# Optimization experiments

Hardware: AMD Instinct MI355X
Metric: run time of the kernel (lower is better)

Reference implementation:

```python
import jax, jax.numpy as jnp
import numpy as np

N_NODES = 100000
N_EDGES = 1600000
F_IN, HID, N_CLS = 64, 64, 40
K = 3  # Chebyshev order


def setup_inputs() -> dict:
    key = jax.random.key(0)
    k = jax.random.split(key, 7)
    x = jax.random.normal(k[0], (N_NODES, F_IN), dtype=jnp.float32)
    edge_index = jax.random.randint(k[1], (2, N_EDGES), 0, N_NODES, dtype=jnp.int32)
    W1 = jax.random.normal(k[2], (K, F_IN, HID), dtype=jnp.float32) * 0.05
    b1 = jax.random.normal(k[3], (HID,), dtype=jnp.float32) * 0.05
    W2 = jax.random.normal(k[4], (K, HID, N_CLS), dtype=jnp.float32) * 0.05
    b2 = jax.random.normal(k[5], (N_CLS,), dtype=jnp.float32) * 0.05
    return {"x": x, "edge_index": edge_index, "W1": W1, "b1": b1, "W2": W2, "b2": b2}


def _norm(edge_index, n):
    # PyG ChebConv with sym normalization and lambda_max=2.0:
    # L_hat edge weight = -deg^{-1/2}[src] * deg^{-1/2}[dst]; self-loop weight 0.
    src, dst = edge_index[0], edge_index[1]
    keep = (src != dst).astype(jnp.float32)  # remove_self_loops
    deg = jax.ops.segment_sum(keep, src, num_segments=n)
    dis = jnp.where(deg > 0, 1.0 / jnp.sqrt(jnp.maximum(deg, 1.0)), 0.0)
    w = -dis[src] * dis[dst] * keep
    return src, dst, w


def _spmm(x, src, dst, w, n):
    # out[i] = sum_{e: dst[e]==i} w[e] * x[src[e]]
    return jax.ops.segment_sum(w[:, None] * x[src], dst, num_segments=n)


def _cheb_conv(x, src, dst, w, W, b, n):
    Tx0 = x
    out = Tx0 @ W[0]
    Tx1 = _spmm(x, src, dst, w, n)
    out = out + Tx1 @ W[1]
    for k in range(2, W.shape[0]):
        Tx2 = 2.0 * _spmm(Tx1, src, dst, w, n) - Tx0
        out = out + Tx2 @ W[k]
        Tx0, Tx1 = Tx1, Tx2
    return out + b


def reference(x, edge_index, W1, b1, W2, b2):
    n = x.shape[0]
    src, dst, w = _norm(edge_index, n)
    h = jax.nn.relu(_cheb_conv(x, src, dst, w, W1, b1, n))
    out = _cheb_conv(h, src, dst, w, W2, b2, n)
    return jax.nn.softmax(out, axis=1)
```

## Files before the change

### kernel.cpp

```cpp
#include <hip/hip_runtime.h>
#include <hip/hip_fp16.h>

#define N_NODES 100000
#define N_EDGES 1600000
#define NCLS 40
#define NBUCK 196
#define CAPE 8960
#define CAPC 10752
#define DUMMY N_NODES

typedef unsigned short u16;
typedef unsigned int u32;
typedef short bf16x8 __attribute__((ext_vector_type(8)));
typedef float f32x4 __attribute__((ext_vector_type(4)));

static inline size_t align256(size_t x) { return (x + 255) & ~(size_t)255; }

__device__ __forceinline__ float bf2f(u16 h) { return __uint_as_float(((u32)h) << 16); }
__device__ __forceinline__ u16 f2bf(float f) {
    u32 u = __float_as_uint(f);
    u += 0x7FFFu + ((u >> 16) & 1u);
    return (u16)(u >> 16);
}
__device__ __forceinline__ u32 pk2(u16 a, u16 b) { return (u32)a | ((u32)b << 16); }
__device__ __forceinline__ u32 pack15(float f) {
    return ((u32)__half_as_ushort(__float2half(f))) & 0x7FFFu;
}
__device__ __forceinline__ float unpack15(u32 bits) {
    return __half2float(__ushort_as_half((u16)bits));
}
__device__ __forceinline__ int perm16(int r, int c8) {
    int base16 = (c8 >> 4) << 4;
    if (r < base16) {
        int b = r >> 4, w = r & 15;
        return (b << 4) + ((w & 1) << 3) + (w >> 1);
    }
    int w = r - base16;
    return base16 + ((w & 1) << 2) + (w >> 1);
}

#define PS_BLOCKS 391
#define CONV_BLOCKS 6250

__global__ __launch_bounds__(256) void pscatter_conv(const int* __restrict__ src,
                                                     const int* __restrict__ dst,
                                                     int* __restrict__ gFillD,
                                                     int* __restrict__ gFillS,
                                                     u32* __restrict__ partD,
                                                     u16* __restrict__ partS,
                                                     const float* __restrict__ x,
                                                     u16* __restrict__ xb) {
    if (blockIdx.x >= PS_BLOCKS) {
        int i = (blockIdx.x - PS_BLOCKS) * 256 + threadIdx.x;
        float4 v = *(const float4*)(x + (size_t)i * 4);
        ushort4 o;
        o.x = f2bf(v.x); o.y = f2bf(v.y); o.z = f2bf(v.z); o.w = f2bf(v.w);
        *(ushort4*)(xb + (size_t)i * 4) = o;
        return;
    }
    __shared__ int histD[NBUCK], histS[NBUCK], chunkD[NBUCK], chunkS[NBUCK];
    int tid = threadIdx.x;
    int base = blockIdx.x * 4096;

    int4 sv[4], dv[4];
#pragma unroll
    for (int j = 0; j < 4; ++j) {
        int idx = base + j * 1024 + tid * 4;
        if (idx < N_EDGES) {
            sv[j] = *(const int4*)(src + idx);
            dv[j] = *(const int4*)(dst + idx);
        } else {
            sv[j] = make_int4(0, 0, 0, 0);
            dv[j] = make_int4(0, 0, 0, 0);
        }
    }

    for (int i = tid; i < NBUCK; i += 256) { histD[i] = 0; histS[i] = 0; }
    __syncthreads();
#pragma unroll
    for (int j = 0; j < 4; ++j)
#pragma unroll
        for (int k = 0; k < 4; ++k) {
            int s = ((const int*)&sv[j])[k], d = ((const int*)&dv[j])[k];
            if (s != d) {
                atomicAdd(&histD[d >> 9], 1);
                atomicAdd(&histS[s >> 9], 1);
            }
        }
    __syncthreads();
    for (int B = tid; B < NBUCK; B += 256) {
        int cD = histD[B];
        chunkD[B] = cD ? atomicAdd(&gFillD[B], cD) : 0;
        int cS = histS[B];
        chunkS[B] = cS ? atomicAdd(&gFillS[B], cS) : 0;
    }
    __syncthreads();
    for (int i = tid; i < NBUCK; i += 256) { histD[i] = 0; histS[i] = 0; }
    __syncthreads();
#pragma unroll
    for (int j = 0; j < 4; ++j)
#pragma unroll
        for (int k = 0; k < 4; ++k) {
            int s = ((const int*)&sv[j])[k], d = ((const int*)&dv[j])[k];
            if (s != d) {
                int bD = d >> 9;
                int r = atomicAdd(&histD[bD], 1);
                int o = chunkD[bD] + r;
                if (o < CAPE) partD[bD * CAPE + o] = ((u32)s << 9) | (u32)(d & 511);
                int bS = s >> 9;
                int r2 = atomicAdd(&histS[bS], 1);
                int o2 = chunkS[bS] + r2;
                if (o2 < CAPE) partS[bS * CAPE + o2] = (u16)(s & 511);
            }
        }
}

__global__ __launch_bounds__(256) void build_dis(const u16* __restrict__ partS,
                                                 const int* __restrict__ gFillS,
                                                 float* __restrict__ dis) {
    __shared__ int cnt[512];
    int tid = threadIdx.x;
    int B = blockIdx.x;
    for (int i = tid; i < 512; i += 256) cnt[i] = 0;
    __syncthreads();
    int nS = min(gFillS[B], CAPE);
    for (int i = tid; i < nS; i += 256) atomicAdd(&cnt[partS[B * CAPE + i]], 1);
    __syncthreads();
    for (int n = tid; n < 512; n += 256) {
        int node = B * 512 + n;
        if (node < N_NODES) {
            int dg = cnt[n];
            dis[node] = dg > 0 ? 1.0f / sqrtf((float)dg) : 0.0f;
        }
    }
}

__global__ __launch_bounds__(256) void build_csr(const u32* __restrict__ partD,
                                                 const int* __restrict__ gFillD,
                                                 const float* __restrict__ dis,
                                                 u32* __restrict__ csr,
                                                 int2* __restrict__ meta) {
    __shared__ int cnt[512], loc[512], rnk[512];
    int tid = threadIdx.x;
    int B = blockIdx.x;
    for (int i = tid; i < 512; i += 256) { cnt[i] = 0; rnk[i] = 0; }
    __syncthreads();
    int nD = min(gFillD[B], CAPE);
    for (int i = tid; i < nD; i += 256) atomicAdd(&cnt[partD[B * CAPE + i] & 511], 1);
    __syncthreads();
    if (tid < 64) {
        int bb = tid * 8, c8[8], mysum = 0;
#pragma unroll
        for (int j = 0; j < 8; ++j) { c8[j] = (cnt[bb + j] + 7) & ~7; mysum += c8[j]; }
        int incl = mysum;
#pragma unroll
        for (int off = 1; off < 64; off <<= 1) {
            int v = __shfl_up(incl, off);
            if (tid >= off) incl += v;
        }
        int run = incl - mysum;
#pragma unroll
        for (int j = 0; j < 8; ++j) { loc[bb + j] = run; run += c8[j]; }
    }
    __syncthreads();
    for (int n = tid; n < 512; n += 256) {
        int node = B * 512 + n;
        if (node < N_NODES) {
            int c = cnt[n], c8 = (c + 7) & ~7;
            meta[node] = make_int2(B * CAPC + loc[n], c);
            for (int e = c; e < c8; ++e)
                csr[B * CAPC + loc[n] + perm16(e, c8)] = (u32)DUMMY;
        }
    }
    for (int i = tid; i < nD; i += 256) {
        u32 p = partD[B * CAPE + i];
        int ln = p & 511;
        u32 s = p >> 9;
        int r = atomicAdd(&rnk[ln], 1);
        int c8 = (cnt[ln] + 7) & ~7;
        int pos = loc[ln] + perm16(r, c8);
        if (pos < CAPC) csr[B * CAPC + pos] = s | (pack15(dis[s]) << 17);
    }
}

__global__ __launch_bounds__(256) void spmm(const u16* __restrict__ in,
                                            const float* __restrict__ dis,
                                            const int2* __restrict__ meta,
                                            const u32* __restrict__ csr,
                                            u16* __restrict__ outhi,
                                            u16* __restrict__ outlo) {
    int node = (blockIdx.x * 256 + threadIdx.x) >> 6;
    int lane = threadIdx.x & 63;
    if (node >= N_NODES) return;
    node = __builtin_amdgcn_readfirstlane(node);
    int2 mt = meta[node];
    int c8 = (mt.y + 7) & ~7;
    const u32* lst = csr + mt.x;
    const u32* in32 = (const u32*)in;
    const int hsel = lane >> 5;
    const int fl = lane & 31;
    float acc0 = 0.0f, acc1 = 0.0f;
    int e = 0;
    for (; e + 16 <= c8; e += 16) {
        const u32* half = lst + e + (hsel << 3);
        uint4 ea = *(const uint4*)half;
        uint4 eb = *(const uint4*)(half + 4);
        u32 e0 = ea.x, e1 = ea.y, e2 = ea.z, e3 = ea.w;
        u32 e4 = eb.x, e5 = eb.y, e6 = eb.z, e7 = eb.w;
        u32 v0 = in32[((e0 & 0x1FFFFu) << 5) + fl];
        u32 v1 = in32[((e1 & 0x1FFFFu) << 5) + fl];
        u32 v2 = in32[((e2 & 0x1FFFFu) << 5) + fl];
        u32 v3 = in32[((e3 & 0x1FFFFu) << 5) + fl];
        u32 v4 = in32[((e4 & 0x1FFFFu) << 5) + fl];
        u32 v5 = in32[((e5 & 0x1FFFFu) << 5) + fl];
        u32 v6 = in32[((e6 & 0x1FFFFu) << 5) + fl];
        u32 v7 = in32[((e7 & 0x1FFFFu) << 5) + fl];
        float w0 = unpack15(e0 >> 17), w1 = unpack15(e1 >> 17);
        float w2 = unpack15(e2 >> 17), w3 = unpack15(e3 >> 17);
        float w4 = unpack15(e4 >> 17), w5 = unpack15(e5 >> 17);
        float w6 = unpack15(e6 >> 17), w7 = unpack15(e7 >> 17);
        acc0 = fmaf(w0, __uint_as_float(v0 << 16), acc0);
        acc1 = fmaf(w0, __uint_as_float(v0 & 0xFFFF0000u), acc1);
        acc0 = fmaf(w1, __uint_as_float(v1 << 16), acc0);
        acc1 = fmaf(w1, __uint_as_float(v1 & 0xFFFF0000u), acc1);
        acc0 = fmaf(w2, __uint_as_float(v2 << 16), acc0);
        acc1 = fmaf(w2, __uint_as_float(v2 & 0xFFFF0000u), acc1);
        acc0 = fmaf(w3, __uint_as_float(v3 << 16), acc0);
        acc1 = fmaf(w3, __uint_as_float(v3 & 0xFFFF0000u), acc1);
        acc0 = fmaf(w4, __uint_as_float(v4 << 16), acc0);
        acc1 = fmaf(w4, __uint_as_float(v4 & 0xFFFF0000u), acc1);
        acc0 = fmaf(w5, __uint_as_float(v5 << 16), acc0);
        acc1 = fmaf(w5, __uint_as_float(v5 & 0xFFFF0000u), acc1);
        acc0 = fmaf(w6, __uint_as_float(v6 << 16), acc0);
        acc1 = fmaf(w6, __uint_as_float(v6 & 0xFFFF0000u), acc1);
        acc0 = fmaf(w7, __uint_as_float(v7 << 16), acc0);
        acc1 = fmaf(w7, __uint_as_float(v7 & 0xFFFF0000u), acc1);
    }
    if (e < c8) {
        const u32* half = lst + e + (hsel << 2);
        uint4 ea = *(const uint4*)half;
        u32 e0 = ea.x, e1 = ea.y, e2 = ea.z, e3 = ea.w;
        u32 v0 = in32[((e0 & 0x1FFFFu) << 5) + fl];
        u32 v1 = in32[((e1 & 0x1FFFFu) << 5) + fl];
        u32 v2 = in32[((e2 & 0x1FFFFu) << 5) + fl];
        u32 v3 = in32[((e3 & 0x1FFFFu) << 5) + fl];
        float w0 = unpack15(e0 >> 17), w1 = unpack15(e1 >> 17);
        float w2 = unpack15(e2 >> 17), w3 = unpack15(e3 >> 17);
        acc0 = fmaf(w0, __uint_as_float(v0 << 16), acc0);
        acc1 = fmaf(w0, __uint_as_float(v0 & 0xFFFF0000u), acc1);
        acc0 = fmaf(w1, __uint_as_float(v1 << 16), acc0);
        acc1 = fmaf(w1, __uint_as_float(v1 & 0xFFFF0000u), acc1);
        acc0 = fmaf(w2, __uint_as_float(v2 << 16), acc0);
        acc1 = fmaf(w2, __uint_as_float(v2 & 0xFFFF0000u), acc1);
        acc0 = fmaf(w3, __uint_as_float(v3 << 16), acc0);
        acc1 = fmaf(w3, __uint_as_float(v3 & 0xFFFF0000u), acc1);
    }
    acc0 += __shfl_xor(acc0, 32);
    acc1 += __shfl_xor(acc1, 32);
    float vd = -dis[node];
    float f0 = vd * acc0, f1 = vd * acc1;
    u32 o32 = ((u32)node << 5) + fl;
    u16 h0 = f2bf(f0), h1 = f2bf(f1);
    if (hsel == 0) {
        ((u32*)outhi)[o32] = pk2(h0, h1);
    } else {
        ((u32*)outlo)[o32] = pk2(f2bf(f0 - bf2f(h0)), f2bf(f1 - bf2f(h1)));
    }
}

#define DGRID 1250
#define DNT 5
#define LSTR 200

__device__ __forceinline__ float foldW(const float* __restrict__ W, int kk, int col,
                                       int ncols) {
    float wv = W[kk * ncols + col];
    if (kk < 64) wv -= W[(kk + 128) * ncols + col];
    else if (kk >= 128) wv += wv;
    return wv;
}

__global__ __launch_bounds__(256) void dense1_mf(const float* __restrict__ x,
                                                 const u16* __restrict__ a1h,
                                                 const u16* __restrict__ a1l,
                                                 const u16* __restrict__ tyh,
                                                 const u16* __restrict__ tyl,
                                                 const float* __restrict__ W,
                                                 const float* __restrict__ bias,
                                                 u16* __restrict__ ohi,
                                                 u16* __restrict__ olo) {
    __shared__ u16 Ah[16 * LSTR], Al[16 * LSTR];
    const int tid = threadIdx.x, wid = tid >> 6, lane = tid & 63;
    const int lrow = lane & 15, lk8 = (lane >> 4) * 8;
    const int col = wid * 16 + lrow;

    bf16x8 wh[6], wl[6];
#pragma unroll
    for (int c = 0; c < 6; ++c) {
        bf16x8 h, l;
#pragma unroll
        for (int i = 0; i < 8; ++i) {
            float wv = foldW(W, c * 32 + lk8 + i, col, 64);
            u16 hb_ = f2bf(wv);
            h[i] = (short)hb_;
            l[i] = (short)f2bf(wv - bf2f(hb_));
        }
        wh[c] = h; wl[c] = l;
    }
    float bv = bias[col];
    const int srow = tid >> 4, sc4 = (tid & 15) * 4;

    for (int t = 0; t < DNT; ++t) {
        int r0 = (blockIdx.x * DNT + t) * 16;
        size_t rb = ((size_t)(r0 + srow) << 6) + sc4;
        {
            float4 v = *(const float4*)&x[rb];
            const float* vp = (const float*)&v;
            ushort4 hv, lv;
#pragma unroll
            for (int i = 0; i < 4; ++i) {
                u16 hb_ = f2bf(vp[i]);
                ((u16*)&hv)[i] = hb_;
                ((u16*)&lv)[i] = f2bf(vp[i] - bf2f(hb_));
            }
            *(ushort4*)&Ah[srow * LSTR + sc4] = hv;
            *(ushort4*)&Al[srow * LSTR + sc4] = lv;
        }
        *(ushort4*)&Ah[srow * LSTR + 64 + sc4] = *(const ushort4*)&a1h[rb];
        *(ushort4*)&Al[srow * LSTR + 64 + sc4] = *(const ushort4*)&a1l[rb];
        *(ushort4*)&Ah[srow * LSTR + 128 + sc4] = *(const ushort4*)&tyh[rb];
        *(ushort4*)&Al[srow * LSTR + 128 + sc4] = *(const ushort4*)&tyl[rb];
        __syncthreads();

        f32x4 acc = {bv, bv, bv, bv};
#pragma unroll
        for (int c = 0; c < 6; ++c) {
            bf16x8 ah = *(const bf16x8*)&Ah[lrow * LSTR + c * 32 + lk8];
            bf16x8 al = *(const bf16x8*)&Al[lrow * LSTR + c * 32 + lk8];
            acc = __builtin_amdgcn_mfma_f32_16x16x32_bf16(ah, wh[c], acc, 0, 0, 0);
            acc = __builtin_amdgcn_mfma_f32_16x16x32_bf16(al, wh[c], acc, 0, 0, 0);
            acc = __builtin_amdgcn_mfma_f32_16x16x32_bf16(ah, wl[c], acc, 0, 0, 0);
        }
        __syncthreads();

#pragma unroll
        for (int j = 0; j < 4; ++j) {
            int row = r0 + (lane >> 4) * 4 + j;
            float v = fmaxf(acc[j], 0.0f);
            u16 hb_ = f2bf(v);
            ohi[((size_t)row << 6) + col] = hb_;
            olo[((size_t)row << 6) + col] = f2bf(v - bf2f(hb_));
        }
    }
}

__global__ __launch_bounds__(256) void dense2_mf(const u16* __restrict__ a0h,
                                                 const u16* __restrict__ a0l,
                                                 const u16* __restrict__ a1h,
                                                 const u16* __restrict__ a1l,
                                                 const u16* __restrict__ tyh,
                                                 const u16* __restrict__ tyl,
                                                 const float* __restrict__ W,
                                                 const float* __restrict__ bias,
                                                 float* __restrict__ out) {
    __shared__ u16 Ah[16 * LSTR], Al[16 * LSTR];
    __shared__ float Ls[16][48];
    const int tid = threadIdx.x, wid = tid >> 6, lane = tid & 63;
    const int lrow = lane & 15, lk8 = (lane >> 4) * 8;
    const int col = wid * 16 + lrow;
    const bool act = (wid < 3);
    const bool cok = act && (col < NCLS);

    bf16x8 wh[6], wl[6];
#pragma unroll
    for (int c = 0; c < 6; ++c) {
        bf16x8 h = 0, l = 0;
        if (cok) {
#pragma unroll
            for (int i = 0; i < 8; ++i) {
                float wv = foldW(W, c * 32 + lk8 + i, col, NCLS);
                u16 hb_ = f2bf(wv);
                h[i] = (short)hb_;
                l[i] = (short)f2bf(wv - bf2f(hb_));
            }
        }
        wh[c] = h; wl[c] = l;
    }
    float bv = cok ? bias[col] : 0.0f;
    const int srow = tid >> 4, sc4 = (tid & 15) * 4;

    for (int t = 0; t < DNT; ++t) {
        int r0 = (blockIdx.x * DNT + t) * 16;
        size_t rb = ((size_t)(r0 + srow) << 6) + sc4;
        *(ushort4*)&Ah[srow * LSTR + sc4] = *(const ushort4*)&a0h[rb];
        *(ushort4*)&Al[srow * LSTR + sc4] = *(const ushort4*)&a0l[rb];
        *(ushort4*)&Ah[srow * LSTR + 64 + sc4] = *(const ushort4*)&a1h[rb];
        *(ushort4*)&Al[srow * LSTR + 64 + sc4] = *(const ushort4*)&a1l[rb];
        *(ushort4*)&Ah[srow * LSTR + 128 + sc4] = *(const ushort4*)&tyh[rb];
        *(ushort4*)&Al[srow * LSTR + 128 + sc4] = *(const ushort4*)&tyl[rb];
        __syncthreads();

        if (act) {
            f32x4 acc = {bv, bv, bv, bv};
#pragma unroll
            for (int c = 0; c < 6; ++c) {
                bf16x8 ah = *(const bf16x8*)&Ah[lrow * LSTR + c * 32 + lk8];
                bf16x8 al = *(const bf16x8*)&Al[lrow * LSTR + c * 32 + lk8];
                acc = __builtin_amdgcn_mfma_f32_16x16x32_bf16(ah, wh[c], acc, 0, 0, 0);
                acc = __builtin_amdgcn_mfma_f32_16x16x32_bf16(al, wh[c], acc, 0, 0, 0);
                acc = __builtin_amdgcn_mfma_f32_16x16x32_bf16(ah, wl[c], acc, 0, 0, 0);
            }
#pragma unroll
            for (int j = 0; j < 4; ++j) Ls[(lane >> 4) * 4 + j][col] = acc[j];
        }
        __syncthreads();

        {
            int row = wid * 4 + (lane >> 4);
            int cg = lane & 15;
            float v0 = Ls[row][cg];
            float v1 = Ls[row][cg + 16];
            float v2 = (cg < 8) ? Ls[row][cg + 32] : -1e30f;
            float m = fmaxf(fmaxf(v0, v1), v2);
#pragma unroll
            for (int o = 8; o; o >>= 1) m = fmaxf(m, __shfl_xor(m, o));
            float e0 = expf(v0 - m), e1 = expf(v1 - m);
            float e2 = (cg < 8) ? expf(v2 - m) : 0.0f;
            float s = e0 + e1 + e2;
#pragma unroll
            for (int o = 8; o; o >>= 1) s += __shfl_xor(s, o);
            float inv = 1.0f / s;
            size_t ob = (size_t)(r0 + row) * NCLS;
            out[ob + cg] = e0 * inv;
            out[ob + cg + 16] = e1 * inv;
            if (cg < 8) out[ob + cg + 32] = e2 * inv;
        }
    }
}


extern "C" void kernel_launch(void* const* d_in, const int* in_sizes, int n_in,
                              void* d_out, int out_size, void* d_ws, size_t ws_size,
                              hipStream_t stream) {
    const float* x = (const float*)d_in[0];
    const int* edge_index = (const int*)d_in[1];
    const float* W1 = (const float*)d_in[2];
    const float* b1 = (const float*)d_in[3];
    const float* W2 = (const float*)d_in[4];
    const float* b2 = (const float*)d_in[5];
    float* out = (float*)d_out;

    const int* src = edge_index;
    const int* dst = edge_index + N_EDGES;

    char* ws = (char*)d_ws;
    size_t off = 0;
    auto carve = [&](size_t bytes) -> void* {
        void* p = ws + off;
        off = align256(off + bytes);
        return p;
    };
    int* gFillD = (int*)carve((size_t)NBUCK * 4);
    int* gFillS = (int*)carve((size_t)NBUCK * 4);
    size_t zero_bytes = off;
    u32* partD = (u32*)carve((size_t)NBUCK * CAPE * 4);
    u16* partS = (u16*)carve((size_t)NBUCK * CAPE * 2);
    u32* csr = (u32*)carve((size_t)NBUCK * CAPC * 4 + 1024);
    int2* meta = (int2*)carve((size_t)N_NODES * 8);
    float* dis = (float*)carve((size_t)(N_NODES + 1) * 4);
    const size_t FB = (size_t)(N_NODES + 1) * 64 * 2;
    u16* xb  = (u16*)carve(FB);
    u16* t1h = (u16*)carve(FB);
    u16* t1l = (u16*)carve(FB);
    u16* tyh = (u16*)carve(FB);
    u16* tyl = (u16*)carve(FB);
    u16* hh  = (u16*)carve(FB);
    u16* hl  = (u16*)carve(FB);

    const int WV = (N_NODES * 64) / 256;

    hipMemsetAsync(d_ws, 0, zero_bytes, stream);

    pscatter_conv<<<PS_BLOCKS + CONV_BLOCKS, 256, 0, stream>>>(src, dst, gFillD, gFillS,
                                                               partD, partS, x, xb);
    build_dis<<<NBUCK, 256, 0, stream>>>(partS, gFillS, dis);
    build_csr<<<NBUCK, 256, 0, stream>>>(partD, gFillD, dis, csr, meta);

    spmm<<<WV, 256, 0, stream>>>(xb, dis, meta, csr, t1h, t1l);
    spmm<<<WV, 256, 0, stream>>>(t1h, dis, meta, csr, tyh, tyl);
    dense1_mf<<<DGRID, 256, 0, stream>>>(x, t1h, t1l, tyh, tyl, W1, b1, hh, hl);

    spmm<<<WV, 256, 0, stream>>>(hh, dis, meta, csr, t1h, t1l);
    spmm<<<WV, 256, 0, stream>>>(t1h, dis, meta, csr, tyh, tyl);
    dense2_mf<<<DGRID, 256, 0, stream>>>(hh, hl, t1h, t1l, tyh, tyl, W2, b2, out);
}
```

Before: 249.6 us.

## Process eight nodes per wavefront with 16-byte gathers in SpMM

SpMM now maps eight destination nodes to each wavefront, with eight lanes per node each gathering a 16-byte slice of the 64-feature bf16 row. Lanes within a group share edge entries through ds_swizzle instead of each loading them. The CSR layout drops the 16-way permutation used by the old split-wavefront scheme and stores edges in plain order. The aim is fewer, wider memory transactions and less per-edge index overhead, at the cost of load imbalance between nodes of different degree sharing one wavefront.

```diff
diff --git a/kernel.cpp b/kernel.cpp
--- a/kernel.cpp
+++ b/kernel.cpp
@@ -29,15 +29,8 @@
 __device__ __forceinline__ float unpack15(u32 bits) {
     return __half2float(__ushort_as_half((u16)bits));
 }
-__device__ __forceinline__ int perm16(int r, int c8) {
-    int base16 = (c8 >> 4) << 4;
-    if (r < base16) {
-        int b = r >> 4, w = r & 15;
-        return (b << 4) + ((w & 1) << 3) + (w >> 1);
-    }
-    int w = r - base16;
-    return base16 + ((w & 1) << 2) + (w >> 1);
-}
+__device__ __forceinline__ float blo(u32 v) { return __uint_as_float(v << 16); }
+__device__ __forceinline__ float bhi(u32 v) { return __uint_as_float(v & 0xFFFF0000u); }
 
 #define PS_BLOCKS 391
 #define CONV_BLOCKS 6250
@@ -168,8 +161,7 @@
         if (node < N_NODES) {
             int c = cnt[n], c8 = (c + 7) & ~7;
             meta[node] = make_int2(B * CAPC + loc[n], c);
-            for (int e = c; e < c8; ++e)
-                csr[B * CAPC + loc[n] + perm16(e, c8)] = (u32)DUMMY;
+            for (int e = c; e < c8; ++e) csr[B * CAPC + loc[n] + e] = (u32)DUMMY;
         }
     }
     for (int i = tid; i < nD; i += 256) {
@@ -177,11 +169,29 @@
         int ln = p & 511;
         u32 s = p >> 9;
         int r = atomicAdd(&rnk[ln], 1);
-        int c8 = (cnt[ln] + 7) & ~7;
-        int pos = loc[ln] + perm16(r, c8);
+        int pos = loc[ln] + r;
         if (pos < CAPC) csr[B * CAPC + pos] = s | (pack15(dis[s]) << 17);
     }
 }
+
+template <int J>
+__device__ __forceinline__ void edge_step(u32 ent, const uint4* __restrict__ in4,
+                                          int p, float* a) {
+    u32 q = (u32)__builtin_amdgcn_ds_swizzle((int)ent, (J << 5) | 0x18);
+    u32 s = q & 0x1FFFFu;
+    float w = unpack15(q >> 17);
+    uint4 v = in4[((size_t)s << 3) + p];
+    a[0] = fmaf(w, blo(v.x), a[0]);
+    a[1] = fmaf(w, bhi(v.x), a[1]);
+    a[2] = fmaf(w, blo(v.y), a[2]);
+    a[3] = fmaf(w, bhi(v.y), a[3]);
+    a[4] = fmaf(w, blo(v.z), a[4]);
+    a[5] = fmaf(w, bhi(v.z), a[5]);
+    a[6] = fmaf(w, blo(v.w), a[6]);
+    a[7] = fmaf(w, bhi(v.w), a[7]);
+}
+
+#define SPMM_BLOCKS 3125
 
 __global__ __launch_bounds__(256) void spmm(const u16* __restrict__ in,
                                             const float* __restrict__ dis,
@@ -189,83 +199,47 @@
                                             const u32* __restrict__ csr,
                                             u16* __restrict__ outhi,
                                             u16* __restrict__ outlo) {
-    int node = (blockIdx.x * 256 + threadIdx.x) >> 6;
-    int lane = threadIdx.x & 63;
-    if (node >= N_NODES) return;
-    node = __builtin_amdgcn_readfirstlane(node);
+    const int tid = threadIdx.x;
+    const int lane = tid & 63;
+    const int gw = blockIdx.x * 4 + (tid >> 6);
+    const int node = gw * 8 + (lane >> 3);
+    const int p = lane & 7;
+
     int2 mt = meta[node];
     int c8 = (mt.y + 7) & ~7;
     const u32* lst = csr + mt.x;
-    const u32* in32 = (const u32*)in;
-    const int hsel = lane >> 5;
-    const int fl = lane & 31;
-    float acc0 = 0.0f, acc1 = 0.0f;
-    int e = 0;
-    for (; e + 16 <= c8; e += 16) {
-        const u32* half = lst + e + (hsel << 3);
-        uint4 ea = *(const uint4*)half;
-        uint4 eb = *(const uint4*)(half + 4);
-        u32 e0 = ea.x, e1 = ea.y, e2 = ea.z, e3 = ea.w;
-        u32 e4 = eb.x, e5 = eb.y, e6 = eb.z, e7 = eb.w;
-        u32 v0 = in32[((e0 & 0x1FFFFu) << 5) + fl];
-        u32 v1 = in32[((e1 & 0x1FFFFu) << 5) + fl];
-        u32 v2 = in32[((e2 & 0x1FFFFu) << 5) + fl];
-        u32 v3 = in32[((e3 & 0x1FFFFu) << 5) + fl];
-        u32 v4 = in32[((e4 & 0x1FFFFu) << 5) + fl];
-        u32 v5 = in32[((e5 & 0x1FFFFu) << 5) + fl];
-        u32 v6 = in32[((e6 & 0x1FFFFu) << 5) + fl];
-        u32 v7 = in32[((e7 & 0x1FFFFu) << 5) + fl];
-        float w0 = unpack15(e0 >> 17), w1 = unpack15(e1 >> 17);
-        float w2 = unpack15(e2 >> 17), w3 = unpack15(e3 >> 17);
-        float w4 = unpack15(e4 >> 17), w5 = unpack15(e5 >> 17);
-        float w6 = unpack15(e6 >> 17), w7 = unpack15(e7 >> 17);
-        acc0 = fmaf(w0, __uint_as_float(v0 << 16), acc0);
-        acc1 = fmaf(w0, __uint_as_float(v0 & 0xFFFF0000u), acc1);
-        acc0 = fmaf(w1, __uint_as_float(v1 << 16), acc0);
-        acc1 = fmaf(w1, __uint_as_float(v1 & 0xFFFF0000u), acc1);
-        acc0 = fmaf(w2, __uint_as_float(v2 << 16), acc0);
-        acc1 = fmaf(w2, __uint_as_float(v2 & 0xFFFF0000u), acc1);
-        acc0 = fmaf(w3, __uint_as_float(v3 << 16), acc0);
-        acc1 = fmaf(w3, __uint_as_float(v3 & 0xFFFF0000u), acc1);
-        acc0 = fmaf(w4, __uint_as_float(v4 << 16), acc0);
-        acc1 = fmaf(w4, __uint_as_float(v4 & 0xFFFF0000u), acc1);
-        acc0 = fmaf(w5, __uint_as_float(v5 << 16), acc0);
-        acc1 = fmaf(w5, __uint_as_float(v5 & 0xFFFF0000u), acc1);
-        acc0 = fmaf(w6, __uint_as_float(v6 << 16), acc0);
-        acc1 = fmaf(w6, __uint_as_float(v6 & 0xFFFF0000u), acc1);
-        acc0 = fmaf(w7, __uint_as_float(v7 << 16), acc0);
-        acc1 = fmaf(w7, __uint_as_float(v7 & 0xFFFF0000u), acc1);
-    }
-    if (e < c8) {
-        const u32* half = lst + e + (hsel << 2);
-        uint4 ea = *(const uint4*)half;
-        u32 e0 = ea.x, e1 = ea.y, e2 = ea.z, e3 = ea.w;
-        u32 v0 = in32[((e0 & 0x1FFFFu) << 5) + fl];
-        u32 v1 = in32[((e1 & 0x1FFFFu) << 5) + fl];
-        u32 v2 = in32[((e2 & 0x1FFFFu) << 5) + fl];
-        u32 v3 = in32[((e3 & 0x1FFFFu) << 5) + fl];
-        float w0 = unpack15(e0 >> 17), w1 = unpack15(e1 >> 17);
-        float w2 = unpack15(e2 >> 17), w3 = unpack15(e3 >> 17);
-        acc0 = fmaf(w0, __uint_as_float(v0 << 16), acc0);
-        acc1 = fmaf(w0, __uint_as_float(v0 & 0xFFFF0000u), acc1);
-        acc0 = fmaf(w1, __uint_as_float(v1 << 16), acc0);
-        acc1 = fmaf(w1, __uint_as_float(v1 & 0xFFFF0000u), acc1);
-        acc0 = fmaf(w2, __uint_as_float(v2 << 16), acc0);
-        acc1 = fmaf(w2, __uint_as_float(v2 & 0xFFFF0000u), acc1);
-        acc0 = fmaf(w3, __uint_as_float(v3 << 16), acc0);
-        acc1 = fmaf(w3, __uint_as_float(v3 & 0xFFFF0000u), acc1);
-    }
-    acc0 += __shfl_xor(acc0, 32);
-    acc1 += __shfl_xor(acc1, 32);
+    const uint4* in4 = (const uint4*)in;
+
+    float a[8] = {0.f, 0.f, 0.f, 0.f, 0.f, 0.f, 0.f, 0.f};
+
+    for (int e = 0; e < c8; e += 8) {
+        u32 ent = lst[e + p];
+        edge_step<0>(ent, in4, p, a);
+        edge_step<1>(ent, in4, p, a);
+        edge_step<2>(ent, in4, p, a);
+        edge_step<3>(ent, in4, p, a);
+        edge_step<4>(ent, in4, p, a);
+        edge_step<5>(ent, in4, p, a);
+        edge_step<6>(ent, in4, p, a);
+        edge_step<7>(ent, in4, p, a);
+    }
+
     float vd = -dis[node];
-    float f0 = vd * acc0, f1 = vd * acc1;
-    u32 o32 = ((u32)node << 5) + fl;
-    u16 h0 = f2bf(f0), h1 = f2bf(f1);
-    if (hsel == 0) {
-        ((u32*)outhi)[o32] = pk2(h0, h1);
-    } else {
-        ((u32*)outlo)[o32] = pk2(f2bf(f0 - bf2f(h0)), f2bf(f1 - bf2f(h1)));
-    }
+    float f0 = vd * a[0], f1 = vd * a[1], f2 = vd * a[2], f3 = vd * a[3];
+    float f4 = vd * a[4], f5 = vd * a[5], f6 = vd * a[6], f7 = vd * a[7];
+
+    u16 h0 = f2bf(f0), h1 = f2bf(f1), h2 = f2bf(f2), h3 = f2bf(f3);
+    u16 h4 = f2bf(f4), h5 = f2bf(f5), h6 = f2bf(f6), h7 = f2bf(f7);
+    uint4 H;
+    H.x = pk2(h0, h1); H.y = pk2(h2, h3); H.z = pk2(h4, h5); H.w = pk2(h6, h7);
+    *((uint4*)((u32*)outhi + (((size_t)node << 5) + (p << 2)))) = H;
+
+    uint4 L;
+    L.x = pk2(f2bf(f0 - bf2f(h0)), f2bf(f1 - bf2f(h1)));
+    L.y = pk2(f2bf(f2 - bf2f(h2)), f2bf(f3 - bf2f(h3)));
+    L.z = pk2(f2bf(f4 - bf2f(h4)), f2bf(f5 - bf2f(h5)));
+    L.w = pk2(f2bf(f6 - bf2f(h6)), f2bf(f7 - bf2f(h7)));
+    *((uint4*)((u32*)outlo + (((size_t)node << 5) + (p << 2)))) = L;
 }
 
 #define DGRID 1250
@@ -477,20 +451,18 @@
     u16* hh  = (u16*)carve(FB);
     u16* hl  = (u16*)carve(FB);
 
-    const int WV = (N_NODES * 64) / 256;
-
-    hipMemsetAsync(d_ws, 0, zero_bytes, stream);
+    (void)hipMemsetAsync(d_ws, 0, zero_bytes, stream);
 
     pscatter_conv<<<PS_BLOCKS + CONV_BLOCKS, 256, 0, stream>>>(src, dst, gFillD, gFillS,
                                                                partD, partS, x, xb);
     build_dis<<<NBUCK, 256, 0, stream>>>(partS, gFillS, dis);
     build_csr<<<NBUCK, 256, 0, stream>>>(partD, gFillD, dis, csr, meta);
 
-    spmm<<<WV, 256, 0, stream>>>(xb, dis, meta, csr, t1h, t1l);
-    spmm<<<WV, 256, 0, stream>>>(t1h, dis, meta, csr, tyh, tyl);
+    spmm<<<SPMM_BLOCKS, 256, 0, stream>>>(xb, dis, meta, csr, t1h, t1l);
+    spmm<<<SPMM_BLOCKS, 256, 0, stream>>>(t1h, dis, meta, csr, tyh, tyl);
     dense1_mf<<<DGRID, 256, 0, stream>>>(x, t1h, t1l, tyh, tyl, W1, b1, hh, hl);
 
-    spmm<<<WV, 256, 0, stream>>>(hh, dis, meta, csr, t1h, t1l);
-    spmm<<<WV, 256, 0, stream>>>(t1h, dis, meta, csr, tyh, tyl);
+    spmm<<<SPMM_BLOCKS, 256, 0, stream>>>(hh, dis, meta, csr, t1h, t1l);
+    spmm<<<SPMM_BLOCKS, 256, 0, stream>>>(t1h, dis, meta, csr, tyh, tyl);
     dense2_mf<<<DGRID, 256, 0, stream>>>(hh, hl, t1h, t1l, tyh, tyl, W2, b2, out);
 }
```

After: 236.5 us. 1.06x faster.
